# Optimization experiments

Measured on AMD Instinct MI355X. Metric: run time of the kernel, lower is better.

Reference implementation:

```python
import jax, jax.numpy as jnp
import numpy as np

H = 16  # hidden size = time_slot(=32) / 2
G = 3 * H  # gate dim (r|z|n), torch gate order


def _gru_dir(x, Wi, Wh, bi, bh, reverse):
    """Single-direction GRU over time. x: [B,T,F]; Wi:[3H,F]; Wh:[3H,H]."""
    xp = jnp.einsum('btf,gf->btg', x, Wi) + bi  # [B,T,3H] input projections, all steps at once
    if reverse:
        xp = xp[:, ::-1]
    xp_t = jnp.swapaxes(xp, 0, 1)  # [T,B,3H]
    h0 = jnp.zeros((x.shape[0], H), x.dtype)

    def step(h, g_x):
        g_h = h @ Wh.T + bh  # [B,3H]
        r = jax.nn.sigmoid(g_x[:, :H] + g_h[:, :H])
        z = jax.nn.sigmoid(g_x[:, H:2 * H] + g_h[:, H:2 * H])
        n = jnp.tanh(g_x[:, 2 * H:] + r * g_h[:, 2 * H:])
        h_new = (1.0 - z) * n + z * h
        return h_new, h_new

    _, ys = jax.lax.scan(step, h0, xp_t)
    ys = jnp.swapaxes(ys, 0, 1)  # [B,T,H]
    if reverse:
        ys = ys[:, ::-1]
    return ys


def _bigru(x, Wi, Wh, bi, bh):
    """Bidirectional GRU layer; params indexed [dir(2), ...]."""
    fwd = _gru_dir(x, Wi[0], Wh[0], bi[0], bh[0], False)
    bwd = _gru_dir(x, Wi[1], Wh[1], bi[1], bh[1], True)
    return jnp.concatenate([fwd, bwd], axis=-1)  # [B,T,2H]


def setup_inputs() -> dict:
    key = jax.random.key(0)
    ks = jax.random.split(key, 12)
    B, T, F_IN, DEPTH, NCLS = 16384, 64, 3, 5, 4
    s = 0.25  # ~1/sqrt(H) torch init scale
    return {
        'x': jax.random.normal(ks[0], (B, T, F_IN), jnp.float32),
        # GRU1: 1 layer, 2 directions, input 3
        'Wi1': jax.random.normal(ks[1], (2, G, F_IN), jnp.float32) * s,
        'Wh1': jax.random.normal(ks[2], (2, G, H), jnp.float32) * s,
        'bi1': jax.random.normal(ks[3], (2, G), jnp.float32) * s,
        'bh1': jax.random.normal(ks[4], (2, G), jnp.float32) * s,
        # GRU5: 5 layers, 2 directions, input 2H=32 every layer
        'Wi5': jax.random.normal(ks[5], (DEPTH, 2, G, 2 * H), jnp.float32) * s,
        'Wh5': jax.random.normal(ks[6], (DEPTH, 2, G, H), jnp.float32) * s,
        'bi5': jax.random.normal(ks[7], (DEPTH, 2, G), jnp.float32) * s,
        'bh5': jax.random.normal(ks[8], (DEPTH, 2, G), jnp.float32) * s,
        # classifier Linear(2H -> num_class)
        'Wc': jax.random.normal(ks[9], (NCLS, 2 * H), jnp.float32) * s,
        'bc': jax.random.normal(ks[10], (NCLS,), jnp.float32) * s,
    }


def reference(x, Wi1, Wh1, bi1, bh1, Wi5, Wh5, bi5, bh5, Wc, bc):
    y = _bigru(x, Wi1, Wh1, bi1, bh1)  # [B,T,2H]
    for l in range(Wi5.shape[0]):  # 5 stacked bi-GRU layers
        y = _bigru(y, Wi5[l], Wh5[l], bi5[l], bh5[l])
    logits = jnp.einsum('btd,cd->btc', y, Wc) + bc  # [B,T,num_class]
    return jax.nn.softmax(logits, axis=2)
```

## Files before the change

### kernel.cpp

```cpp
#include <hip/hip_runtime.h>

#define T 64
#define F_IN 3
#define H 16
#define G 48
#define D2 32
#define DEPTH 5
#define NCLS 4
#define L2E 1.44269504f

#define YST 32
#define YSB 2048
#define HZ_ZOFF 64

typedef _Float16 half8 __attribute__((ext_vector_type(8)));
typedef float f32x4v __attribute__((ext_vector_type(4)));

__device__ __forceinline__ float fexp2(float x) { return __builtin_amdgcn_exp2f(x); }
__device__ __forceinline__ float frcp(float x)  { return __builtin_amdgcn_rcpf(x); }

__global__ __launch_bounds__(64, 3) void bigru_all(
    const float* __restrict__ x,
    const float* __restrict__ Wi1, const float* __restrict__ Wh1,
    const float* __restrict__ bi1, const float* __restrict__ bh1,
    const float* __restrict__ Wi5, const float* __restrict__ Wh5,
    const float* __restrict__ bi5, const float* __restrict__ bh5,
    const float* __restrict__ Wc,  const float* __restrict__ bc,
    float* __restrict__ out)
{
    __shared__ __align__(16) _Float16 yb[2 * YSB];
    __shared__ __align__(16) _Float16 hzb[80];

    const int lane = threadIdx.x;
    const int j15  = lane & 15;
    const int quad = lane >> 4;
    const int lb   = quad & 1;
    const int dir  = quad >> 1;
    const bool isf = (dir == 0);

    hzb[lane] = (_Float16)0.0f;
    if (lane < 16) hzb[64 + lane] = (_Float16)0.0f;

    const int  job_a  = j15 >> 2;
    const bool avalid = ((j15 >> 3) == 0) ? (quad < 2) : (quad >= 2);
    const _Float16* aptr = hzb + (avalid ? (job_a * 16 + (quad & 1) * 8) : HZ_ZOFF);

    const int ystep = isf ? YST : -YST;
    const f32x4v zC = {0.f, 0.f, 0.f, 0.f};
    const int klo = (quad & 1) * 8;
    const int bdir = (quad < 2) ? 0 : 1;

    float hj;

    {
        half8 whB[3];
        {
            const float* wsrc = Wh1 + bdir * (G * H);
            #pragma unroll
            for (int g = 0; g < 3; ++g) {
                const float scale = (g == 2) ? (-2.0f * L2E) : L2E;
                const float* w = wsrc + (g * 16 + j15) * H + klo;
                half8 hv;
                #pragma unroll
                for (int i = 0; i < 8; ++i) hv[i] = (_Float16)(scale * w[i]);
                whB[g] = hv;
            }
        }
        float wi[3][F_IN];
        float bir[3], bhn2;
        {
            const float* Wi = Wi1 + dir * (G * F_IN);
            const float* bi = bi1 + dir * G;
            const float* bh = bh1 + dir * G;
            #pragma unroll
            for (int g = 0; g < 3; ++g) {
                const float scale = (g == 2) ? (-2.0f * L2E) : L2E;
                int row = g * H + j15;
                #pragma unroll
                for (int k = 0; k < F_IN; ++k) wi[g][k] = scale * Wi[row * F_IN + k];
                bir[g] = scale * bi[row] + ((g < 2) ? (L2E * bh[row]) : 0.0f);
            }
            bhn2 = -2.0f * L2E * bh[2 * H + j15];
        }
        const f32x4v cN = {bhn2, bhn2, bhn2, bhn2};
        hj = 0.0f;

        const float* xg = x + (size_t)blockIdx.x * (2 * T * F_IN) + (size_t)lb * (T * F_IN);
        _Float16* yw = yb + lb * YSB + (isf ? 0 : (T - 1)) * YST + dir * H + j15;

        #pragma unroll 4
        for (int s = 0; s < T; ++s) {
            int t = isf ? s : (T - 1 - s);
            const float* xp = xg + t * F_IN;
            float x0 = xp[0], x1 = xp[1], x2 = xp[2];
            float gxr = fmaf(wi[0][2], x2, fmaf(wi[0][1], x1, fmaf(wi[0][0], x0, bir[0])));
            float gxz = fmaf(wi[1][2], x2, fmaf(wi[1][1], x1, fmaf(wi[1][0], x0, bir[1])));
            float gxn = fmaf(wi[2][2], x2, fmaf(wi[2][1], x1, fmaf(wi[2][0], x0, bir[2])));
            half8 a = *(const half8*)aptr;
            f32x4v d0 = __builtin_amdgcn_mfma_f32_16x16x32_f16(a, whB[0], zC, 0, 0, 0);
            f32x4v d1 = __builtin_amdgcn_mfma_f32_16x16x32_f16(a, whB[1], zC, 0, 0, 0);
            f32x4v d2 = __builtin_amdgcn_mfma_f32_16x16x32_f16(a, whB[2], cN, 0, 0, 0);
            float av = gxr + d0[0];
            float bv = gxz + d1[0];
            float Er = fexp2(fminf(58.f, -av));
            float rg = frcp(1.0f + Er);
            float c2 = fmaf(rg, d2[0], gxn);
            float Ez = fexp2(fminf(58.f, -bv));
            float Ec = fexp2(fminf(63.f, c2));
            float num = fmaf(hj - Ez, Ec, hj + Ez);
            float den = (1.0f + Ec) * (1.0f + Ez);
            float hn = num * frcp(den);
            hj = hn;
            _Float16 hh = (_Float16)hn;
            hzb[lane] = hh;
            *yw = hh;
            yw += ystep;
        }
    }

    #pragma unroll 1
    for (int l = 0; l < DEPTH; ++l) {
        half8 bflo[3], bfhi[3];
        #pragma unroll
        for (int g = 0; g < 3; ++g) {
            const float scale = (g == 2) ? (-2.0f * L2E) : L2E;
            const float* w = Wi5 + ((size_t)(l * 2 + bdir) * G + g * 16 + j15) * D2;
            half8 lo, hi;
            #pragma unroll
            for (int i = 0; i < 8; ++i) {
                lo[i] = (_Float16)(scale * w[klo + i]);
                hi[i] = (_Float16)(scale * w[16 + klo + i]);
            }
            bflo[g] = lo;
            bfhi[g] = hi;
        }
        half8 whB[3];
        {
            const float* wsrc = Wh5 + ((size_t)(l * 2) + bdir) * G * H;
            #pragma unroll
            for (int g = 0; g < 3; ++g) {
                const float scale = (g == 2) ? (-2.0f * L2E) : L2E;
                const float* w = wsrc + (g * 16 + j15) * H + klo;
                half8 hv;
                #pragma unroll
                for (int i = 0; i < 8; ++i) hv[i] = (_Float16)(scale * w[i]);
                whB[g] = hv;
            }
        }
        float bib0, bib1, bib2, bhn2;
        {
            const float* biL = bi5 + (l * 2 + dir) * G;
            const float* bhL = bh5 + (l * 2 + dir) * G;
            bib0 = L2E * (biL[j15]     + bhL[j15]);
            bib1 = L2E * (biL[H + j15] + bhL[H + j15]);
            bib2 = -2.0f * L2E * biL[2 * H + j15];
            bhn2 = -2.0f * L2E * bhL[2 * H + j15];
        }
        const f32x4v cR  = {bib0, bib0, bib0, bib0};
        const f32x4v cZ  = {bib1, bib1, bib1, bib1};
        const f32x4v cNx = {bib2, bib2, bib2, bib2};
        const f32x4v cN  = {bhn2, bhn2, bhn2, bhn2};

        hj = 0.0f;
        hzb[lane] = (_Float16)0.0f;

        const bool fsel = (j15 < 8);
        const int  lb_a = (j15 >> 2) & 1;
        const int  tl_a = j15 & 3;
        const bool axv  = fsel ? (quad < 2) : (quad >= 2);

        unsigned int ypk[16];

        #pragma unroll
        for (int c = 0; c < 8; ++c) {
            const int trow = fsel ? (4 * c + tl_a) : (T - 1 - 4 * c - tl_a);
            const _Float16* abase = yb + lb_a * YSB + trow * YST;
            half8 alo = *(const half8*)(axv ? (abase + klo)      : (hzb + HZ_ZOFF));
            half8 ahi = *(const half8*)(axv ? (abase + 16 + klo) : (hzb + HZ_ZOFF));
            f32x4v c0 = __builtin_amdgcn_mfma_f32_16x16x32_f16(alo, bflo[0], cR, 0, 0, 0);
            f32x4v c1 = __builtin_amdgcn_mfma_f32_16x16x32_f16(alo, bflo[1], cZ, 0, 0, 0);
            f32x4v c2g = __builtin_amdgcn_mfma_f32_16x16x32_f16(alo, bflo[2], cNx, 0, 0, 0);
            c0  = __builtin_amdgcn_mfma_f32_16x16x32_f16(ahi, bfhi[0], c0, 0, 0, 0);
            c1  = __builtin_amdgcn_mfma_f32_16x16x32_f16(ahi, bfhi[1], c1, 0, 0, 0);
            c2g = __builtin_amdgcn_mfma_f32_16x16x32_f16(ahi, bfhi[2], c2g, 0, 0, 0);

            #pragma unroll
            for (int s = 0; s < 4; ++s) {
                half8 a = *(const half8*)aptr;
                f32x4v d0 = __builtin_amdgcn_mfma_f32_16x16x32_f16(a, whB[0], zC, 0, 0, 0);
                f32x4v d1 = __builtin_amdgcn_mfma_f32_16x16x32_f16(a, whB[1], zC, 0, 0, 0);
                f32x4v d2 = __builtin_amdgcn_mfma_f32_16x16x32_f16(a, whB[2], cN, 0, 0, 0);
                float av = c0[s] + d0[0];
                float bv = c1[s] + d1[0];
                float Er = fexp2(fminf(58.f, -av));
                float rg = frcp(1.0f + Er);
                float cc = fmaf(rg, d2[0], c2g[s]);
                float Ez = fexp2(fminf(58.f, -bv));
                float Ec = fexp2(fminf(63.f, cc));
                float num = fmaf(hj - Ez, Ec, hj + Ez);
                float den = (1.0f + Ec) * (1.0f + Ez);
                float hn = num * frcp(den);
                hj = hn;
                _Float16 hh = (_Float16)hn;
                hzb[lane] = hh;
                unsigned int hb16 = (unsigned int)__builtin_bit_cast(unsigned short, hh);
                if (s & 1) ypk[2 * c + (s >> 1)] |= hb16 << 16;
                else       ypk[2 * c + (s >> 1)]  = hb16;
            }
        }

        {
            _Float16* yw = yb + lb * YSB + (isf ? 32 : 31) * YST + dir * H + j15;
            #pragma unroll 1
            for (int c = 8; c < 16; ++c) {
                const int trow = fsel ? (4 * c + tl_a) : (T - 1 - 4 * c - tl_a);
                const _Float16* abase = yb + lb_a * YSB + trow * YST;
                half8 alo = *(const half8*)(axv ? (abase + klo)      : (hzb + HZ_ZOFF));
                half8 ahi = *(const half8*)(axv ? (abase + 16 + klo) : (hzb + HZ_ZOFF));
                f32x4v c0 = __builtin_amdgcn_mfma_f32_16x16x32_f16(alo, bflo[0], cR, 0, 0, 0);
                f32x4v c1 = __builtin_amdgcn_mfma_f32_16x16x32_f16(alo, bflo[1], cZ, 0, 0, 0);
                f32x4v c2g = __builtin_amdgcn_mfma_f32_16x16x32_f16(alo, bflo[2], cNx, 0, 0, 0);
                c0  = __builtin_amdgcn_mfma_f32_16x16x32_f16(ahi, bfhi[0], c0, 0, 0, 0);
                c1  = __builtin_amdgcn_mfma_f32_16x16x32_f16(ahi, bfhi[1], c1, 0, 0, 0);
                c2g = __builtin_amdgcn_mfma_f32_16x16x32_f16(ahi, bfhi[2], c2g, 0, 0, 0);

                #pragma unroll
                for (int s = 0; s < 4; ++s) {
                    half8 a = *(const half8*)aptr;
                    f32x4v d0 = __builtin_amdgcn_mfma_f32_16x16x32_f16(a, whB[0], zC, 0, 0, 0);
                    f32x4v d1 = __builtin_amdgcn_mfma_f32_16x16x32_f16(a, whB[1], zC, 0, 0, 0);
                    f32x4v d2 = __builtin_amdgcn_mfma_f32_16x16x32_f16(a, whB[2], cN, 0, 0, 0);
                    float av = c0[s] + d0[0];
                    float bv = c1[s] + d1[0];
                    float Er = fexp2(fminf(58.f, -av));
                    float rg = frcp(1.0f + Er);
                    float cc = fmaf(rg, d2[0], c2g[s]);
                    float Ez = fexp2(fminf(58.f, -bv));
                    float Ec = fexp2(fminf(63.f, cc));
                    float num = fmaf(hj - Ez, Ec, hj + Ez);
                    float den = (1.0f + Ec) * (1.0f + Ez);
                    float hn = num * frcp(den);
                    hj = hn;
                    _Float16 hh = (_Float16)hn;
                    hzb[lane] = hh;
                    *yw = hh;
                    yw += ystep;
                }
            }
        }

        {
            _Float16* yw = yb + lb * YSB + (isf ? 0 : (T - 1)) * YST + dir * H + j15;
            #pragma unroll
            for (int i = 0; i < 16; ++i) {
                unsigned int v = ypk[i];
                *yw = __builtin_bit_cast(_Float16, (unsigned short)(v & 0xffffu));
                yw += ystep;
                *yw = __builtin_bit_cast(_Float16, (unsigned short)(v >> 16));
                yw += ystep;
            }
        }
    }

    #pragma unroll
    for (int i = 0; i < 2; ++i) {
        int idx = lane + i * 64;
        int bb  = idx >> 6;
        int t   = idx & 63;
        const _Float16* yrow = yb + bb * YSB + t * YST;
        float yv[D2];
        #pragma unroll
        for (int k8 = 0; k8 < 4; ++k8) {
            half8 v = *(const half8*)(yrow + k8 * 8);
            #pragma unroll
            for (int i8 = 0; i8 < 8; ++i8) yv[k8 * 8 + i8] = (float)v[i8];
        }
        float lg[NCLS];
        #pragma unroll
        for (int c = 0; c < NCLS; ++c) {
            const float* wc = Wc + c * D2;
            float acc = bc[c];
            #pragma unroll
            for (int k = 0; k < D2; ++k) acc = fmaf(wc[k], yv[k], acc);
            lg[c] = acc;
        }
        float m = fmaxf(fmaxf(lg[0], lg[1]), fmaxf(lg[2], lg[3]));
        float e0 = __expf(lg[0] - m), e1 = __expf(lg[1] - m);
        float e2 = __expf(lg[2] - m), e3 = __expf(lg[3] - m);
        float inv = frcp(e0 + e1 + e2 + e3);
        size_t bglob = (size_t)blockIdx.x * 2 + bb;
        float4 o;
        o.x = e0 * inv; o.y = e1 * inv; o.z = e2 * inv; o.w = e3 * inv;
        ((float4*)out)[bglob * T + t] = o;
    }
}

extern "C" void kernel_launch(void* const* d_in, const int* in_sizes, int n_in,
                              void* d_out, int out_size, void* d_ws, size_t ws_size,
                              hipStream_t stream) {
    const float* x   = (const float*)d_in[0];
    const float* Wi1 = (const float*)d_in[1];
    const float* Wh1 = (const float*)d_in[2];
    const float* bi1 = (const float*)d_in[3];
    const float* bh1 = (const float*)d_in[4];
    const float* Wi5 = (const float*)d_in[5];
    const float* Wh5 = (const float*)d_in[6];
    const float* bi5 = (const float*)d_in[7];
    const float* bh5 = (const float*)d_in[8];
    const float* Wc  = (const float*)d_in[9];
    const float* bc  = (const float*)d_in[10];
    float* out = (float*)d_out;

    const int B = in_sizes[0] / (T * F_IN);
    dim3 grid(B / 2), block(64);
    hipLaunchKernelGGL(bigru_all, grid, block, 0, stream,
                       x, Wi1, Wh1, bi1, bh1, Wi5, Wh5, bi5, bh5, Wc, bc, out);
}
```

Baseline: 347.8 us.

## Fold input projections into recurrent MFMA accumulators and prefetch next chunk operands

```diff
diff --git a/kernel.cpp b/kernel.cpp
--- a/kernel.cpp
+++ b/kernel.cpp
@@ -19,7 +19,7 @@
 __device__ __forceinline__ float fexp2(float x) { return __builtin_amdgcn_exp2f(x); }
 __device__ __forceinline__ float frcp(float x)  { return __builtin_amdgcn_rcpf(x); }
 
-__global__ __launch_bounds__(64, 3) void bigru_all(
+__global__ __launch_bounds__(64, 4) void bigru_all(
     const float* __restrict__ x,
     const float* __restrict__ Wi1, const float* __restrict__ Wh1,
     const float* __restrict__ bi1, const float* __restrict__ bh1,
@@ -46,7 +46,6 @@
     const _Float16* aptr = hzb + (avalid ? (job_a * 16 + (quad & 1) * 8) : HZ_ZOFF);
 
     const int ystep = isf ? YST : -YST;
-    const f32x4v zC = {0.f, 0.f, 0.f, 0.f};
     const int klo = (quad & 1) * 8;
     const int bdir = (quad < 2) ? 0 : 1;
 
@@ -85,36 +84,65 @@
         const f32x4v cN = {bhn2, bhn2, bhn2, bhn2};
         hj = 0.0f;
 
-        const float* xg = x + (size_t)blockIdx.x * (2 * T * F_IN) + (size_t)lb * (T * F_IN);
+        const float* xw = x + (size_t)blockIdx.x * (2 * T * F_IN);
+        int xip = lb * (T * F_IN) + (isf ? 0 : (T - 1) * F_IN);
+        const int xst = isf ? F_IN : -F_IN;
         _Float16* yw = yb + lb * YSB + (isf ? 0 : (T - 1)) * YST + dir * H + j15;
 
-        #pragma unroll 4
-        for (int s = 0; s < T; ++s) {
-            int t = isf ? s : (T - 1 - s);
-            const float* xp = xg + t * F_IN;
-            float x0 = xp[0], x1 = xp[1], x2 = xp[2];
-            float gxr = fmaf(wi[0][2], x2, fmaf(wi[0][1], x1, fmaf(wi[0][0], x0, bir[0])));
-            float gxz = fmaf(wi[1][2], x2, fmaf(wi[1][1], x1, fmaf(wi[1][0], x0, bir[1])));
-            float gxn = fmaf(wi[2][2], x2, fmaf(wi[2][1], x1, fmaf(wi[2][0], x0, bir[2])));
-            half8 a = *(const half8*)aptr;
-            f32x4v d0 = __builtin_amdgcn_mfma_f32_16x16x32_f16(a, whB[0], zC, 0, 0, 0);
-            f32x4v d1 = __builtin_amdgcn_mfma_f32_16x16x32_f16(a, whB[1], zC, 0, 0, 0);
-            f32x4v d2 = __builtin_amdgcn_mfma_f32_16x16x32_f16(a, whB[2], cN, 0, 0, 0);
-            float av = gxr + d0[0];
-            float bv = gxz + d1[0];
-            float Er = fexp2(fminf(58.f, -av));
-            float rg = frcp(1.0f + Er);
-            float c2 = fmaf(rg, d2[0], gxn);
-            float Ez = fexp2(fminf(58.f, -bv));
-            float Ec = fexp2(fminf(63.f, c2));
-            float num = fmaf(hj - Ez, Ec, hj + Ez);
-            float den = (1.0f + Ec) * (1.0f + Ez);
-            float hn = num * frcp(den);
-            hj = hn;
-            _Float16 hh = (_Float16)hn;
-            hzb[lane] = hh;
-            *yw = hh;
-            yw += ystep;
+        float xr[12], xn[12];
+        #pragma unroll
+        for (int g2 = 0; g2 < 4; ++g2) {
+            xr[3 * g2 + 0] = xw[xip + 0];
+            xr[3 * g2 + 1] = xw[xip + 1];
+            xr[3 * g2 + 2] = xw[xip + 2];
+            xip += xst;
+        }
+        #pragma unroll
+        for (int c = 0; c < 16; ++c) {
+            if (c < 15) {
+                #pragma unroll
+                for (int g2 = 0; g2 < 4; ++g2) {
+                    xn[3 * g2 + 0] = xw[xip + 0];
+                    xn[3 * g2 + 1] = xw[xip + 1];
+                    xn[3 * g2 + 2] = xw[xip + 2];
+                    xip += xst;
+                }
+            }
+            f32x4v c0, c1, c2g;
+            #pragma unroll
+            for (int s = 0; s < 4; ++s) {
+                float x0 = xr[3 * s], x1 = xr[3 * s + 1], x2 = xr[3 * s + 2];
+                c0[s]  = fmaf(wi[0][2], x2, fmaf(wi[0][1], x1, fmaf(wi[0][0], x0, bir[0])));
+                c1[s]  = fmaf(wi[1][2], x2, fmaf(wi[1][1], x1, fmaf(wi[1][0], x0, bir[1])));
+                c2g[s] = fmaf(wi[2][2], x2, fmaf(wi[2][1], x1, fmaf(wi[2][0], x0, bir[2])));
+            }
+            #pragma unroll
+            for (int s = 0; s < 4; ++s) {
+                half8 a = *(const half8*)aptr;
+                f32x4v d0 = __builtin_amdgcn_mfma_f32_16x16x32_f16(a, whB[0], c0, 0, 0, 0);
+                f32x4v d1 = __builtin_amdgcn_mfma_f32_16x16x32_f16(a, whB[1], c1, 0, 0, 0);
+                f32x4v d2 = __builtin_amdgcn_mfma_f32_16x16x32_f16(a, whB[2], cN, 0, 0, 0);
+                float Er = fexp2(-d0[s]);
+                float Ez = fexp2(-d1[s]);
+                float rg = frcp(1.0f + Er);
+                float dz = 1.0f + Ez;
+                float tA = hj - Ez;
+                float tB = hj + Ez;
+                float cc = fmaf(rg, d2[0], c2g[s]);
+                float Ec = fexp2(cc);
+                float num = fmaf(tA, Ec, tB);
+                float den = fmaf(dz, Ec, dz);
+                float hn = num * frcp(den);
+                hj = hn;
+                _Float16 hh = (_Float16)hn;
+                hzb[lane] = hh;
+                *yw = hh;
+                yw += ystep;
+            }
+            if (c < 15) {
+                #pragma unroll
+                for (int q2 = 0; q2 < 12; ++q2) xr[q2] = xn[q2];
+            }
         }
     }
 
@@ -168,37 +196,50 @@
         const int  lb_a = (j15 >> 2) & 1;
         const int  tl_a = j15 & 3;
         const bool axv  = fsel ? (quad < 2) : (quad >= 2);
+        const _Float16* zp = hzb + HZ_ZOFF;
 
         unsigned int ypk[16];
 
+        half8 alo, ahi, nlo, nhi;
+        {
+            const int trow0 = fsel ? tl_a : (T - 1 - tl_a);
+            const _Float16* ab = yb + lb_a * YSB + trow0 * YST;
+            alo = *(const half8*)(axv ? (ab + klo)      : zp);
+            ahi = *(const half8*)(axv ? (ab + 16 + klo) : zp);
+        }
+
         #pragma unroll
         for (int c = 0; c < 8; ++c) {
-            const int trow = fsel ? (4 * c + tl_a) : (T - 1 - 4 * c - tl_a);
-            const _Float16* abase = yb + lb_a * YSB + trow * YST;
-            half8 alo = *(const half8*)(axv ? (abase + klo)      : (hzb + HZ_ZOFF));
-            half8 ahi = *(const half8*)(axv ? (abase + 16 + klo) : (hzb + HZ_ZOFF));
-            f32x4v c0 = __builtin_amdgcn_mfma_f32_16x16x32_f16(alo, bflo[0], cR, 0, 0, 0);
-            f32x4v c1 = __builtin_amdgcn_mfma_f32_16x16x32_f16(alo, bflo[1], cZ, 0, 0, 0);
+            f32x4v c0  = __builtin_amdgcn_mfma_f32_16x16x32_f16(alo, bflo[0], cR, 0, 0, 0);
+            f32x4v c1  = __builtin_amdgcn_mfma_f32_16x16x32_f16(alo, bflo[1], cZ, 0, 0, 0);
             f32x4v c2g = __builtin_amdgcn_mfma_f32_16x16x32_f16(alo, bflo[2], cNx, 0, 0, 0);
             c0  = __builtin_amdgcn_mfma_f32_16x16x32_f16(ahi, bfhi[0], c0, 0, 0, 0);
             c1  = __builtin_amdgcn_mfma_f32_16x16x32_f16(ahi, bfhi[1], c1, 0, 0, 0);
             c2g = __builtin_amdgcn_mfma_f32_16x16x32_f16(ahi, bfhi[2], c2g, 0, 0, 0);
 
+            {
+                const int trow = fsel ? (4 * (c + 1) + tl_a) : (T - 1 - 4 * (c + 1) - tl_a);
+                const _Float16* ab = yb + lb_a * YSB + trow * YST;
+                nlo = *(const half8*)(axv ? (ab + klo)      : zp);
+                nhi = *(const half8*)(axv ? (ab + 16 + klo) : zp);
+            }
+
             #pragma unroll
             for (int s = 0; s < 4; ++s) {
                 half8 a = *(const half8*)aptr;
-                f32x4v d0 = __builtin_amdgcn_mfma_f32_16x16x32_f16(a, whB[0], zC, 0, 0, 0);
-                f32x4v d1 = __builtin_amdgcn_mfma_f32_16x16x32_f16(a, whB[1], zC, 0, 0, 0);
+                f32x4v d0 = __builtin_amdgcn_mfma_f32_16x16x32_f16(a, whB[0], c0, 0, 0, 0);
+                f32x4v d1 = __builtin_amdgcn_mfma_f32_16x16x32_f16(a, whB[1], c1, 0, 0, 0);
                 f32x4v d2 = __builtin_amdgcn_mfma_f32_16x16x32_f16(a, whB[2], cN, 0, 0, 0);
-                float av = c0[s] + d0[0];
-                float bv = c1[s] + d1[0];
-                float Er = fexp2(fminf(58.f, -av));
+                float Er = fexp2(-d0[s]);
+                float Ez = fexp2(-d1[s]);
                 float rg = frcp(1.0f + Er);
+                float dz = 1.0f + Ez;
+                float tA = hj - Ez;
+                float tB = hj + Ez;
                 float cc = fmaf(rg, d2[0], c2g[s]);
-                float Ez = fexp2(fminf(58.f, -bv));
-                float Ec = fexp2(fminf(63.f, cc));
-                float num = fmaf(hj - Ez, Ec, hj + Ez);
-                float den = (1.0f + Ec) * (1.0f + Ez);
+                float Ec = fexp2(cc);
+                float num = fmaf(tA, Ec, tB);
+                float den = fmaf(dz, Ec, dz);
                 float hn = num * frcp(den);
                 hj = hn;
                 _Float16 hh = (_Float16)hn;
@@ -207,44 +248,54 @@
                 if (s & 1) ypk[2 * c + (s >> 1)] |= hb16 << 16;
                 else       ypk[2 * c + (s >> 1)]  = hb16;
             }
+            alo = nlo;
+            ahi = nhi;
         }
 
         {
             _Float16* yw = yb + lb * YSB + (isf ? 32 : 31) * YST + dir * H + j15;
-            #pragma unroll 1
+            #pragma unroll
             for (int c = 8; c < 16; ++c) {
-                const int trow = fsel ? (4 * c + tl_a) : (T - 1 - 4 * c - tl_a);
-                const _Float16* abase = yb + lb_a * YSB + trow * YST;
-                half8 alo = *(const half8*)(axv ? (abase + klo)      : (hzb + HZ_ZOFF));
-                half8 ahi = *(const half8*)(axv ? (abase + 16 + klo) : (hzb + HZ_ZOFF));
-                f32x4v c0 = __builtin_amdgcn_mfma_f32_16x16x32_f16(alo, bflo[0], cR, 0, 0, 0);
-                f32x4v c1 = __builtin_amdgcn_mfma_f32_16x16x32_f16(alo, bflo[1], cZ, 0, 0, 0);
+                f32x4v c0  = __builtin_amdgcn_mfma_f32_16x16x32_f16(alo, bflo[0], cR, 0, 0, 0);
+                f32x4v c1  = __builtin_amdgcn_mfma_f32_16x16x32_f16(alo, bflo[1], cZ, 0, 0, 0);
                 f32x4v c2g = __builtin_amdgcn_mfma_f32_16x16x32_f16(alo, bflo[2], cNx, 0, 0, 0);
                 c0  = __builtin_amdgcn_mfma_f32_16x16x32_f16(ahi, bfhi[0], c0, 0, 0, 0);
                 c1  = __builtin_amdgcn_mfma_f32_16x16x32_f16(ahi, bfhi[1], c1, 0, 0, 0);
                 c2g = __builtin_amdgcn_mfma_f32_16x16x32_f16(ahi, bfhi[2], c2g, 0, 0, 0);
 
+                if (c < 15) {
+                    const int trow = fsel ? (4 * (c + 1) + tl_a) : (T - 1 - 4 * (c + 1) - tl_a);
+                    const _Float16* ab = yb + lb_a * YSB + trow * YST;
+                    nlo = *(const half8*)(axv ? (ab + klo)      : zp);
+                    nhi = *(const half8*)(axv ? (ab + 16 + klo) : zp);
+                }
+
                 #pragma unroll
                 for (int s = 0; s < 4; ++s) {
                     half8 a = *(const half8*)aptr;
-                    f32x4v d0 = __builtin_amdgcn_mfma_f32_16x16x32_f16(a, whB[0], zC, 0, 0, 0);
-                    f32x4v d1 = __builtin_amdgcn_mfma_f32_16x16x32_f16(a, whB[1], zC, 0, 0, 0);
+                    f32x4v d0 = __builtin_amdgcn_mfma_f32_16x16x32_f16(a, whB[0], c0, 0, 0, 0);
+                    f32x4v d1 = __builtin_amdgcn_mfma_f32_16x16x32_f16(a, whB[1], c1, 0, 0, 0);
                     f32x4v d2 = __builtin_amdgcn_mfma_f32_16x16x32_f16(a, whB[2], cN, 0, 0, 0);
-                    float av = c0[s] + d0[0];
-                    float bv = c1[s] + d1[0];
-                    float Er = fexp2(fminf(58.f, -av));
+                    float Er = fexp2(-d0[s]);
+                    float Ez = fexp2(-d1[s]);
                     float rg = frcp(1.0f + Er);
+                    float dz = 1.0f + Ez;
+                    float tA = hj - Ez;
+                    float tB = hj + Ez;
                     float cc = fmaf(rg, d2[0], c2g[s]);
-                    float Ez = fexp2(fminf(58.f, -bv));
-                    float Ec = fexp2(fminf(63.f, cc));
-                    float num = fmaf(hj - Ez, Ec, hj + Ez);
-                    float den = (1.0f + Ec) * (1.0f + Ez);
+                    float Ec = fexp2(cc);
+                    float num = fmaf(tA, Ec, tB);
+                    float den = fmaf(dz, Ec, dz);
                     float hn = num * frcp(den);
                     hj = hn;
                     _Float16 hh = (_Float16)hn;
                     hzb[lane] = hh;
                     *yw = hh;
                     yw += ystep;
+                }
+                if (c < 15) {
+                    alo = nlo;
+                    ahi = nhi;
                 }
             }
         }
```

Result: slower. 509.6 us (+46.5%).
